# Kernel tuning notes

Hardware: AMD Instinct MI355X
Metric: run time of the kernel (lower is better)

The kernel has to match this reference:

```python
import jax, jax.numpy as jnp
import numpy as np

D_MODEL = 1024
H = 16
D_H = D_MODEL // H


def setup_inputs() -> dict:
    key = jax.random.key(0)
    ks = jax.random.split(key, 10)
    B, T_dec, T_enc = 2, 2048, 2048
    s = 1.0 / np.sqrt(D_MODEL)
    return {
        "tgt": jax.random.normal(ks[0], (B, T_dec, D_MODEL), jnp.float32),
        "memory": jax.random.normal(ks[1], (B, T_enc, D_MODEL), jnp.float32),
        "W_q": jax.random.normal(ks[2], (D_MODEL, D_MODEL), jnp.float32) * s,
        "b_q": jnp.zeros((D_MODEL,), jnp.float32),
        "W_k": jax.random.normal(ks[3], (D_MODEL, D_MODEL), jnp.float32) * s,
        "b_k": jnp.zeros((D_MODEL,), jnp.float32),
        "W_v": jax.random.normal(ks[4], (D_MODEL, D_MODEL), jnp.float32) * s,
        "b_v": jnp.zeros((D_MODEL,), jnp.float32),
        "W_o": jax.random.normal(ks[5], (D_MODEL, D_MODEL), jnp.float32) * s,
        "b_o": jnp.zeros((D_MODEL,), jnp.float32),
    }


def reference(tgt, memory, W_q, b_q, W_k, b_k, W_v, b_v, W_o, b_o):
    B, T_dec, _ = tgt.shape
    T_enc = memory.shape[1]
    # Projections (nn.Linear: x @ W^T + b; here W stored as (in,out) so x @ W + b)
    Q = tgt @ W_q + b_q          # (B, T_dec, d_model)
    K = memory @ W_k + b_k       # (B, T_enc, d_model)
    V = memory @ W_v + b_v       # (B, T_enc, d_model)
    # split heads: (B, h, T, d_h)
    Q = Q.reshape(B, T_dec, H, D_H).transpose(0, 2, 1, 3)
    K = K.reshape(B, T_enc, H, D_H).transpose(0, 2, 1, 3)
    V = V.reshape(B, T_enc, H, D_H).transpose(0, 2, 1, 3)
    # scores (B, h, T_dec, T_enc)
    S = jnp.einsum("bhqd,bhkd->bhqk", Q, K) / jnp.sqrt(jnp.float32(D_H)).astype(Q.dtype)
    A = jax.nn.softmax(S, axis=-1)
    Y = jnp.einsum("bhqk,bhkd->bhqd", A, V)
    Y = Y.transpose(0, 2, 1, 3).reshape(B, T_dec, D_MODEL)
    return Y @ W_o + b_o
```

## Files before the change

kernel.cpp:

```cpp
#include <hip/hip_runtime.h>
#include <hip/hip_bf16.h>
#include <stdint.h>

typedef unsigned short u16;
typedef __attribute__((ext_vector_type(8))) short bf16x8;
typedef __attribute__((ext_vector_type(4))) short bf16x4;
typedef __attribute__((ext_vector_type(4))) float f32x4;

__device__ __forceinline__ float bf2f(u16 u) {
    union { unsigned int i; float f; } v; v.i = ((unsigned int)u) << 16; return v.f;
}
__device__ __forceinline__ u16 f2bf(float f) {
    union { float f; unsigned int i; } v; v.f = f;
    unsigned int x = v.i;
    return (u16)((x + 0x7fffu + ((x >> 16) & 1u)) >> 16);
}
__device__ __forceinline__ unsigned fbits(float f) {
    union { float f; unsigned int i; } v; v.f = f; return v.i;
}
__device__ __forceinline__ void async16(const void* g, void* lds) {
    __builtin_amdgcn_global_load_lds((const __attribute__((address_space(1))) void*)g,
                                     (__attribute__((address_space(3))) void*)lds,
                                     16, 0, 0);
}

#define QSCALE 0.18033688f

__global__ __launch_bounds__(256) void prep(
    const float* __restrict__ tgt, const float* __restrict__ mem,
    const float* __restrict__ Wq, const float* __restrict__ Wk,
    const float* __restrict__ Wv, const float* __restrict__ Wo,
    u16* __restrict__ Wt, u16* __restrict__ tgtb, u16* __restrict__ memb)
{
    __shared__ u16 tile[64][65];
    const int id = blockIdx.x;
    const int tid = threadIdx.x;
    if (id < 1024) {
        const int z = id >> 8;
        const float* in = (z == 0) ? Wq : (z == 1) ? Wk : (z == 2) ? Wv : Wo;
        u16* out = Wt + (size_t)z * 1048576;
        const int k0 = (id & 15) * 64, n0 = ((id >> 4) & 15) * 64;
        const int r = tid >> 2, c0 = (tid & 3) << 4;
#pragma unroll
        for (int i = 0; i < 4; ++i) {
            float4 v = *(const float4*)&in[(size_t)(k0 + r) * 1024 + n0 + c0 + i * 4];
            tile[c0 + i * 4 + 0][r] = f2bf(v.x);
            tile[c0 + i * 4 + 1][r] = f2bf(v.y);
            tile[c0 + i * 4 + 2][r] = f2bf(v.z);
            tile[c0 + i * 4 + 3][r] = f2bf(v.w);
        }
        __syncthreads();
#pragma unroll
        for (int i = 0; i < 2; ++i) {
            bf16x8 v;
#pragma unroll
            for (int j = 0; j < 8; ++j) v[j] = (short)tile[r][c0 + i * 8 + j];
            *(bf16x8*)&out[(size_t)(n0 + r) * 1024 + k0 + c0 + i * 8] = v;
        }
    } else {
        size_t i = ((size_t)(id - 1024) * 256 + tid) * 8;
        float4 a0 = *(const float4*)&tgt[i];
        float4 a1 = *(const float4*)&tgt[i + 4];
        float4 b0 = *(const float4*)&mem[i];
        float4 b1 = *(const float4*)&mem[i + 4];
        bf16x8 va, vb;
        va[0] = (short)f2bf(a0.x); va[1] = (short)f2bf(a0.y);
        va[2] = (short)f2bf(a0.z); va[3] = (short)f2bf(a0.w);
        va[4] = (short)f2bf(a1.x); va[5] = (short)f2bf(a1.y);
        va[6] = (short)f2bf(a1.z); va[7] = (short)f2bf(a1.w);
        vb[0] = (short)f2bf(b0.x); vb[1] = (short)f2bf(b0.y);
        vb[2] = (short)f2bf(b0.z); vb[3] = (short)f2bf(b0.w);
        vb[4] = (short)f2bf(b1.x); vb[5] = (short)f2bf(b1.y);
        vb[6] = (short)f2bf(b1.z); vb[7] = (short)f2bf(b1.w);
        *(bf16x8*)&tgtb[i] = va;
        *(bf16x8*)&memb[i] = vb;
    }
}

__global__ __launch_bounds__(256) void gemm_qkv(
    const u16* __restrict__ tgtb, const u16* __restrict__ memb,
    const u16* __restrict__ Wt,
    const float* __restrict__ bq, const float* __restrict__ bk, const float* __restrict__ bv,
    u16* __restrict__ Qb, u16* __restrict__ Kb, u16* __restrict__ Vtb)
{
    __shared__ __align__(16) u16 sA[128 * 32];
    __shared__ __align__(16) u16 sB[128 * 32];
    const int z = blockIdx.z;
    const u16* A = (z == 0) ? tgtb : memb;
    const u16* Bt = Wt + (size_t)z * 1048576;
    const float* bias = (z == 0) ? bq : (z == 1) ? bk : bv;

    const int tid = threadIdx.x;
    const int wave = tid >> 6, lane = tid & 63;
    const int quad = lane >> 4, l16 = lane & 15;
    const int m0 = blockIdx.x * 128, n0 = blockIdx.y * 128;
    const int wm = (wave & 1) * 64, wn = (wave >> 1) * 64;
    const int sw = (quad ^ ((l16 >> 1) & 3)) << 3;

    f32x4 acc[4][4] = {};

    for (int k0 = 0; k0 < 1024; k0 += 32) {
        __syncthreads();
#pragma unroll
        for (int r = 0; r < 2; ++r) {
            int c = tid + r * 256;
            int g = (c & 3) ^ ((c >> 3) & 3);
            const u16* gA = A + (size_t)(m0 + (c >> 2)) * 1024 + k0 + g * 8;
            async16(gA, (char*)sA + r * 4096 + wave * 1024);
            const u16* gB = Bt + (size_t)(n0 + (c >> 2)) * 1024 + k0 + g * 8;
            async16(gB, (char*)sB + r * 4096 + wave * 1024);
        }
        __syncthreads();
        bf16x8 af[4], bfr[4];
#pragma unroll
        for (int i = 0; i < 4; ++i) {
            af[i]  = *(const bf16x8*)&sA[(wm + i * 16 + l16) * 32 + sw];
            bfr[i] = *(const bf16x8*)&sB[(wn + i * 16 + l16) * 32 + sw];
        }
#pragma unroll
        for (int i = 0; i < 4; ++i)
#pragma unroll
            for (int j = 0; j < 4; ++j)
                acc[i][j] = __builtin_amdgcn_mfma_f32_16x16x32_bf16(af[i], bfr[j], acc[i][j], 0, 0, 0);
    }

    if (z == 2) {
#pragma unroll
        for (int j = 0; j < 4; ++j) {
            int n = n0 + wn + j * 16 + l16;
            float bb = bias[n];
            int d = n & 63;
#pragma unroll
            for (int i = 0; i < 4; ++i) {
                int mb = m0 + wm + i * 16 + quad * 4;
                int bh = (mb >> 11) * 16 + (n >> 6);
                bf16x4 pk;
#pragma unroll
                for (int r = 0; r < 4; ++r) pk[r] = (short)f2bf(acc[i][j][r] + bb);
                *(bf16x4*)&Vtb[(size_t)bh * 131072 + (size_t)d * 2048 + (mb & 2047)] = pk;
            }
        }
    } else {
        u16* C = (z == 0) ? Qb : Kb;
        const float scl = (z == 0) ? QSCALE : 1.0f;
#pragma unroll
        for (int j = 0; j < 4; ++j) {
            int n = n0 + wn + j * 16 + l16;
            float bb = bias[n];
#pragma unroll
            for (int i = 0; i < 4; ++i) {
                int mb = m0 + wm + i * 16 + quad * 4;
#pragma unroll
                for (int r = 0; r < 4; ++r)
                    C[(size_t)(mb + r) * 1024 + n] = f2bf((acc[i][j][r] + bb) * scl);
            }
        }
    }
}

__global__ __launch_bounds__(256) void gemm_out(
    const u16* __restrict__ A, const u16* __restrict__ Bt,
    const float* __restrict__ bias, float* __restrict__ C)
{
    __shared__ __align__(16) u16 sA[64 * 32];
    __shared__ __align__(16) u16 sB[128 * 32];
    const int tid = threadIdx.x;
    const int wave = tid >> 6, lane = tid & 63;
    const int quad = lane >> 4, l16 = lane & 15;
    const int m0 = blockIdx.x * 64, n0 = blockIdx.y * 128;
    const int wm = (wave & 1) * 32, wn = (wave >> 1) * 64;
    const int sw = (quad ^ ((l16 >> 1) & 3)) << 3;
    f32x4 acc[2][4] = {};

    for (int k0 = 0; k0 < 1024; k0 += 32) {
        __syncthreads();
        {
            int c = tid;
            int g = (c & 3) ^ ((c >> 3) & 3);
            const u16* gA = A + (size_t)(m0 + (c >> 2)) * 1024 + k0 + g * 8;
            async16(gA, (char*)sA + wave * 1024);
        }
#pragma unroll
        for (int r = 0; r < 2; ++r) {
            int c = tid + r * 256;
            int g = (c & 3) ^ ((c >> 3) & 3);
            const u16* gB = Bt + (size_t)(n0 + (c >> 2)) * 1024 + k0 + g * 8;
            async16(gB, (char*)sB + r * 4096 + wave * 1024);
        }
        __syncthreads();
        bf16x8 af[2], bfr[4];
#pragma unroll
        for (int i = 0; i < 2; ++i)
            af[i] = *(const bf16x8*)&sA[(wm + i * 16 + l16) * 32 + sw];
#pragma unroll
        for (int j = 0; j < 4; ++j)
            bfr[j] = *(const bf16x8*)&sB[(wn + j * 16 + l16) * 32 + sw];
#pragma unroll
        for (int i = 0; i < 2; ++i)
#pragma unroll
            for (int j = 0; j < 4; ++j)
                acc[i][j] = __builtin_amdgcn_mfma_f32_16x16x32_bf16(af[i], bfr[j], acc[i][j], 0, 0, 0);
    }
#pragma unroll
    for (int j = 0; j < 4; ++j) {
        int n = n0 + wn + j * 16 + l16;
        float bb = bias[n];
#pragma unroll
        for (int i = 0; i < 2; ++i) {
            int mb = m0 + wm + i * 16 + quad * 4;
#pragma unroll
            for (int r = 0; r < 4; ++r)
                C[(size_t)(mb + r) * 1024 + n] = acc[i][j][r] + bb;
        }
    }
}

__global__ __launch_bounds__(512, 4) void attn_kernel(
    const u16* __restrict__ Q,
    const u16* __restrict__ K,
    const u16* __restrict__ Vt,
    u16* __restrict__ Y)
{
    __shared__ __align__(16) u16 sK[2][4096];
    __shared__ __align__(16) u16 sV[2][4096];

    const int tid = threadIdx.x;
    const int wave = tid >> 6, lane = tid & 63;
    const int quad = lane >> 4, l16 = lane & 15;

    const int bidx = blockIdx.x;
    const int bh = (bidx & 7) * 4 + ((bidx >> 3) & 3);
    const int qt = bidx >> 5;
    const int b = bh >> 4, h = bh & 15;
    const size_t qrow0 = (size_t)b * 2048 + qt * 128;
    const int st = ((qt << 1) | (bh & 1)) & 31;

    const size_t qrow = qrow0 + wave * 16 + l16;
    bf16x8 qf0 = *(const bf16x8*)&Q[qrow * 1024 + h * 64 + quad * 8];
    bf16x8 qf1 = *(const bf16x8*)&Q[qrow * 1024 + h * 64 + 32 + quad * 8];

    f32x4 oacc[4] = {};
    float rowacc = 0.0f;

    const u16* Kbase = K + (size_t)b * 2048 * 1024 + h * 64;
    const u16* Vbase = Vt + (size_t)bh * 131072;

    const int x7 = l16 & 7;
    int koff[4][2], voff[4][4];
#pragma unroll
    for (int ks = 0; ks < 4; ++ks)
#pragma unroll
        for (int kf = 0; kf < 2; ++kf)
            koff[ks][kf] = ((ks * 16 + l16) * 8 + ((kf * 4 + quad) ^ x7)) * 8;
#pragma unroll
    for (int mt = 0; mt < 4; ++mt)
#pragma unroll
        for (int ks = 0; ks < 4; ++ks)
            voff[mt][ks] = ((mt * 16 + l16) * 8 + ((ks * 2 + (quad >> 1)) ^ x7)) * 8 + (quad & 1) * 4;

    const int srow = tid >> 3;
    const int g = (tid & 7) ^ (srow & 7);

#define STAGE(kv0, buf)                                                          \
    {                                                                            \
        async16(Kbase + (size_t)((kv0) + srow) * 1024 + g * 8,                   \
                (char*)&sK[buf][0] + wave * 1024);                               \
        async16(Vbase + (size_t)srow * 2048 + (kv0) + g * 8,                     \
                (char*)&sV[buf][0] + wave * 1024);                               \
    }

    STAGE((st & 31) * 64, 0);

    for (int i = 0; i < 32; ++i) {
        __syncthreads();
        if (i < 31) {
            int kvn = ((st + i + 1) & 31) * 64;
            STAGE(kvn, (i + 1) & 1);
        }
        const u16* kb = &sK[i & 1][0];
        const u16* vb = &sV[i & 1][0];
#pragma unroll
        for (int ks = 0; ks < 4; ++ks) {
            bf16x8 kf0 = *(const bf16x8*)&kb[koff[ks][0]];
            bf16x8 kf1 = *(const bf16x8*)&kb[koff[ks][1]];
            f32x4 s = {0.f, 0.f, 0.f, 0.f};
            s = __builtin_amdgcn_mfma_f32_16x16x32_bf16(kf0, qf0, s, 0, 0, 0);
            s = __builtin_amdgcn_mfma_f32_16x16x32_bf16(kf1, qf1, s, 0, 0, 0);
            float p0 = __builtin_amdgcn_exp2f(s[0]);
            float p1 = __builtin_amdgcn_exp2f(s[1]);
            float p2 = __builtin_amdgcn_exp2f(s[2]);
            float p3 = __builtin_amdgcn_exp2f(s[3]);
            rowacc += (p0 + p1) + (p2 + p3);
            unsigned lo = __builtin_amdgcn_perm(fbits(p1) + 0x8000u, fbits(p0) + 0x8000u, 0x07060302u);
            unsigned hi = __builtin_amdgcn_perm(fbits(p3) + 0x8000u, fbits(p2) + 0x8000u, 0x07060302u);
            union { unsigned u[2]; bf16x4 v; } pku;
            pku.u[0] = lo; pku.u[1] = hi;
#pragma unroll
            for (int mt = 0; mt < 4; ++mt) {
                bf16x4 vv = *(const bf16x4*)&vb[voff[mt][ks]];
                oacc[mt] = __builtin_amdgcn_mfma_f32_16x16x16bf16_1k(vv, pku.v, oacc[mt], 0, 0, 0);
            }
        }
    }
#undef STAGE

    rowacc += __shfl_xor(rowacc, 16, 64);
    rowacc += __shfl_xor(rowacc, 32, 64);
    const float inv = 1.0f / rowacc;

#pragma unroll
    for (int mt = 0; mt < 4; ++mt) {
        bf16x4 o;
#pragma unroll
        for (int r = 0; r < 4; ++r) o[r] = (short)f2bf(oacc[mt][r] * inv);
        *(bf16x4*)&Y[qrow * 1024 + h * 64 + mt * 16 + quad * 4] = o;
    }
}

extern "C" void kernel_launch(void* const* d_in, const int* in_sizes, int n_in,
                              void* d_out, int out_size, void* d_ws, size_t ws_size,
                              hipStream_t stream) {
    const float* tgt = (const float*)d_in[0];
    const float* mem = (const float*)d_in[1];
    const float* Wq  = (const float*)d_in[2];
    const float* bq  = (const float*)d_in[3];
    const float* Wk  = (const float*)d_in[4];
    const float* bk  = (const float*)d_in[5];
    const float* Wv  = (const float*)d_in[6];
    const float* bv  = (const float*)d_in[7];
    const float* Wo  = (const float*)d_in[8];
    const float* bo  = (const float*)d_in[9];

    u16* ws = (u16*)d_ws;
    const size_t SZ = 4194304;
    u16* Wt   = ws;
    u16* tgtb = ws + 4 * SZ;
    u16* memb = tgtb + SZ;
    u16* Qb   = memb + SZ;
    u16* Kb   = Qb + SZ;
    u16* Vtb  = Kb + SZ;
    u16* Yb   = Vtb + SZ;
    float* out = (float*)d_out;

    prep<<<dim3(3072), 256, 0, stream>>>(tgt, mem, Wq, Wk, Wv, Wo, Wt, tgtb, memb);
    gemm_qkv<<<dim3(32, 8, 3), 256, 0, stream>>>(tgtb, memb, Wt, bq, bk, bv, Qb, Kb, Vtb);
    attn_kernel<<<dim3(512), 512, 0, stream>>>(Qb, Kb, Vtb, Yb);
    gemm_out<<<dim3(64, 8), 256, 0, stream>>>(Yb, Wt + 3 * (size_t)1048576, bo, out);
}
```

Before: 224.0 us.

## Process two query row tiles per wave in attention to reuse K/V fragments

The attention block drops from 8 waves to 4, and each wave now handles 32 query rows (two 16-row tiles) instead of 16. Each K and V fragment read from LDS feeds two MFMAs, which halves LDS read traffic per unit of compute. Staging is split into two passes per thread so the 64-row K/V tiles are still fully loaded. The cost is more registers per wave (doubled accumulators and Q fragments) and fewer waves per block, so there is less latency hiding.

```diff
diff --git a/kernel.cpp b/kernel.cpp
--- a/kernel.cpp
+++ b/kernel.cpp
@@ -215,7 +215,7 @@
     }
 }
 
-__global__ __launch_bounds__(512, 4) void attn_kernel(
+__global__ __launch_bounds__(256, 4) void attn_kernel(
     const u16* __restrict__ Q,
     const u16* __restrict__ K,
     const u16* __restrict__ Vt,
@@ -235,41 +235,41 @@
     const size_t qrow0 = (size_t)b * 2048 + qt * 128;
     const int st = ((qt << 1) | (bh & 1)) & 31;
 
-    const size_t qrow = qrow0 + wave * 16 + l16;
-    bf16x8 qf0 = *(const bf16x8*)&Q[qrow * 1024 + h * 64 + quad * 8];
-    bf16x8 qf1 = *(const bf16x8*)&Q[qrow * 1024 + h * 64 + 32 + quad * 8];
-
-    f32x4 oacc[4] = {};
-    float rowacc = 0.0f;
+    const size_t qrowA = qrow0 + wave * 32 + l16;
+    const size_t qrowB = qrowA + 16;
+    bf16x8 qA0 = *(const bf16x8*)&Q[qrowA * 1024 + h * 64 + quad * 8];
+    bf16x8 qA1 = *(const bf16x8*)&Q[qrowA * 1024 + h * 64 + 32 + quad * 8];
+    bf16x8 qB0 = *(const bf16x8*)&Q[qrowB * 1024 + h * 64 + quad * 8];
+    bf16x8 qB1 = *(const bf16x8*)&Q[qrowB * 1024 + h * 64 + 32 + quad * 8];
+
+    f32x4 oA[4] = {}, oB[4] = {};
+    float rowA = 0.0f, rowB = 0.0f;
 
     const u16* Kbase = K + (size_t)b * 2048 * 1024 + h * 64;
     const u16* Vbase = Vt + (size_t)bh * 131072;
 
     const int x7 = l16 & 7;
-    int koff[4][2], voff[4][4];
+    int koff[2], voff[4];
+#pragma unroll
+    for (int kf = 0; kf < 2; ++kf)
+        koff[kf] = (l16 * 8 + ((kf * 4 + quad) ^ x7)) * 8;
 #pragma unroll
     for (int ks = 0; ks < 4; ++ks)
-#pragma unroll
-        for (int kf = 0; kf < 2; ++kf)
-            koff[ks][kf] = ((ks * 16 + l16) * 8 + ((kf * 4 + quad) ^ x7)) * 8;
-#pragma unroll
-    for (int mt = 0; mt < 4; ++mt)
-#pragma unroll
-        for (int ks = 0; ks < 4; ++ks)
-            voff[mt][ks] = ((mt * 16 + l16) * 8 + ((ks * 2 + (quad >> 1)) ^ x7)) * 8 + (quad & 1) * 4;
-
-    const int srow = tid >> 3;
-    const int g = (tid & 7) ^ (srow & 7);
-
-#define STAGE(kv0, buf)                                                          \
-    {                                                                            \
-        async16(Kbase + (size_t)((kv0) + srow) * 1024 + g * 8,                   \
-                (char*)&sK[buf][0] + wave * 1024);                               \
-        async16(Vbase + (size_t)srow * 2048 + (kv0) + g * 8,                     \
-                (char*)&sV[buf][0] + wave * 1024);                               \
-    }
-
-    STAGE((st & 31) * 64, 0);
+        voff[ks] = (l16 * 8 + ((ks * 2 + (quad >> 1)) ^ x7)) * 8 + (quad & 1) * 4;
+
+#define STAGE1(kv0, buf, r)                                                   \
+    {                                                                         \
+        int c = tid + (r) * 256;                                              \
+        int srow = c >> 3;                                                    \
+        int g = (c & 7) ^ (srow & 7);                                         \
+        async16(Kbase + (size_t)((kv0) + srow) * 1024 + g * 8,                \
+                (char*)&sK[buf][0] + (r) * 4096 + wave * 1024);               \
+        async16(Vbase + (size_t)srow * 2048 + (kv0) + g * 8,                  \
+                (char*)&sV[buf][0] + (r) * 4096 + wave * 1024);               \
+    }
+#define STAGE(kv0, buf) STAGE1(kv0, buf, 0) STAGE1(kv0, buf, 1)
+
+    STAGE(st * 64, 0);
 
     for (int i = 0; i < 32; ++i) {
         __syncthreads();
@@ -281,39 +281,59 @@
         const u16* vb = &sV[i & 1][0];
 #pragma unroll
         for (int ks = 0; ks < 4; ++ks) {
-            bf16x8 kf0 = *(const bf16x8*)&kb[koff[ks][0]];
-            bf16x8 kf1 = *(const bf16x8*)&kb[koff[ks][1]];
-            f32x4 s = {0.f, 0.f, 0.f, 0.f};
-            s = __builtin_amdgcn_mfma_f32_16x16x32_bf16(kf0, qf0, s, 0, 0, 0);
-            s = __builtin_amdgcn_mfma_f32_16x16x32_bf16(kf1, qf1, s, 0, 0, 0);
-            float p0 = __builtin_amdgcn_exp2f(s[0]);
-            float p1 = __builtin_amdgcn_exp2f(s[1]);
-            float p2 = __builtin_amdgcn_exp2f(s[2]);
-            float p3 = __builtin_amdgcn_exp2f(s[3]);
-            rowacc += (p0 + p1) + (p2 + p3);
-            unsigned lo = __builtin_amdgcn_perm(fbits(p1) + 0x8000u, fbits(p0) + 0x8000u, 0x07060302u);
-            unsigned hi = __builtin_amdgcn_perm(fbits(p3) + 0x8000u, fbits(p2) + 0x8000u, 0x07060302u);
-            union { unsigned u[2]; bf16x4 v; } pku;
-            pku.u[0] = lo; pku.u[1] = hi;
+            bf16x8 kf0 = *(const bf16x8*)&kb[ks * 1024 + koff[0]];
+            bf16x8 kf1 = *(const bf16x8*)&kb[ks * 1024 + koff[1]];
+            f32x4 sA = {0.f, 0.f, 0.f, 0.f};
+            f32x4 sB = {0.f, 0.f, 0.f, 0.f};
+            sA = __builtin_amdgcn_mfma_f32_16x16x32_bf16(kf0, qA0, sA, 0, 0, 0);
+            sB = __builtin_amdgcn_mfma_f32_16x16x32_bf16(kf0, qB0, sB, 0, 0, 0);
+            sA = __builtin_amdgcn_mfma_f32_16x16x32_bf16(kf1, qA1, sA, 0, 0, 0);
+            sB = __builtin_amdgcn_mfma_f32_16x16x32_bf16(kf1, qB1, sB, 0, 0, 0);
+            float a0 = __builtin_amdgcn_exp2f(sA[0]);
+            float a1 = __builtin_amdgcn_exp2f(sA[1]);
+            float a2 = __builtin_amdgcn_exp2f(sA[2]);
+            float a3 = __builtin_amdgcn_exp2f(sA[3]);
+            float b0 = __builtin_amdgcn_exp2f(sB[0]);
+            float b1 = __builtin_amdgcn_exp2f(sB[1]);
+            float b2 = __builtin_amdgcn_exp2f(sB[2]);
+            float b3 = __builtin_amdgcn_exp2f(sB[3]);
+            rowA += (a0 + a1) + (a2 + a3);
+            rowB += (b0 + b1) + (b2 + b3);
+            unsigned loA = __builtin_amdgcn_perm(fbits(a1) + 0x8000u, fbits(a0) + 0x8000u, 0x07060302u);
+            unsigned hiA = __builtin_amdgcn_perm(fbits(a3) + 0x8000u, fbits(a2) + 0x8000u, 0x07060302u);
+            unsigned loB = __builtin_amdgcn_perm(fbits(b1) + 0x8000u, fbits(b0) + 0x8000u, 0x07060302u);
+            unsigned hiB = __builtin_amdgcn_perm(fbits(b3) + 0x8000u, fbits(b2) + 0x8000u, 0x07060302u);
+            union { unsigned u[2]; bf16x4 v; } pA, pB;
+            pA.u[0] = loA; pA.u[1] = hiA;
+            pB.u[0] = loB; pB.u[1] = hiB;
 #pragma unroll
             for (int mt = 0; mt < 4; ++mt) {
-                bf16x4 vv = *(const bf16x4*)&vb[voff[mt][ks]];
-                oacc[mt] = __builtin_amdgcn_mfma_f32_16x16x16bf16_1k(vv, pku.v, oacc[mt], 0, 0, 0);
+                bf16x4 vv = *(const bf16x4*)&vb[mt * 1024 + voff[ks]];
+                oA[mt] = __builtin_amdgcn_mfma_f32_16x16x16bf16_1k(vv, pA.v, oA[mt], 0, 0, 0);
+                oB[mt] = __builtin_amdgcn_mfma_f32_16x16x16bf16_1k(vv, pB.v, oB[mt], 0, 0, 0);
             }
         }
     }
 #undef STAGE
-
-    rowacc += __shfl_xor(rowacc, 16, 64);
-    rowacc += __shfl_xor(rowacc, 32, 64);
-    const float inv = 1.0f / rowacc;
+#undef STAGE1
+
+    rowA += __shfl_xor(rowA, 16, 64);
+    rowA += __shfl_xor(rowA, 32, 64);
+    rowB += __shfl_xor(rowB, 16, 64);
+    rowB += __shfl_xor(rowB, 32, 64);
+    const float invA = 1.0f / rowA;
+    const float invB = 1.0f / rowB;
 
 #pragma unroll
     for (int mt = 0; mt < 4; ++mt) {
-        bf16x4 o;
-#pragma unroll
-        for (int r = 0; r < 4; ++r) o[r] = (short)f2bf(oacc[mt][r] * inv);
-        *(bf16x4*)&Y[qrow * 1024 + h * 64 + mt * 16 + quad * 4] = o;
+        bf16x4 oa, ob;
+#pragma unroll
+        for (int r = 0; r < 4; ++r) {
+            oa[r] = (short)f2bf(oA[mt][r] * invA);
+            ob[r] = (short)f2bf(oB[mt][r] * invB);
+        }
+        *(bf16x4*)&Y[qrowA * 1024 + h * 64 + mt * 16 + quad * 4] = oa;
+        *(bf16x4*)&Y[qrowB * 1024 + h * 64 + mt * 16 + quad * 4] = ob;
     }
 }
 
@@ -344,6 +364,6 @@
 
     prep<<<dim3(3072), 256, 0, stream>>>(tgt, mem, Wq, Wk, Wv, Wo, Wt, tgtb, memb);
     gemm_qkv<<<dim3(32, 8, 3), 256, 0, stream>>>(tgtb, memb, Wt, bq, bk, bv, Qb, Kb, Vtb);
-    attn_kernel<<<dim3(512), 512, 0, stream>>>(Qb, Kb, Vtb, Yb);
+    attn_kernel<<<dim3(512), 256, 0, stream>>>(Qb, Kb, Vtb, Yb);
     gemm_out<<<dim3(64, 8), 256, 0, stream>>>(Yb, Wt + 3 * (size_t)1048576, bo, out);
 }
```

Measured after the change: 219.7 us. About the same (-2.0%).
